# Optimization experiments

Hardware: AMD Instinct MI355X
Metric: run time of the kernel (lower is better)

## Reference

```python
import jax, jax.numpy as jnp
import numpy as np

NUM_HIDDEN = 128
NUM_IN = 256
NUM_HEADS = 4
B, T, N, K = 4, 32, 96, 30


def setup_inputs() -> dict:
    key = jax.random.key(0)
    ks = jax.random.split(key, 7)
    return {
        "h_V": jax.random.normal(ks[0], (B, T, N, NUM_HIDDEN), dtype=jnp.float32),
        "h_EV": jax.random.normal(ks[1], (B, T, N, K, NUM_IN), dtype=jnp.float32),
        "mask_attend": jax.random.randint(ks[2], (B, T, N, K), 0, 2, dtype=jnp.int32),
        "Wq": jax.random.normal(ks[3], (NUM_HIDDEN, NUM_HIDDEN), dtype=jnp.float32) / np.sqrt(NUM_HIDDEN),
        "Wk": jax.random.normal(ks[4], (NUM_IN, NUM_HIDDEN), dtype=jnp.float32) / np.sqrt(NUM_IN),
        "Wv": jax.random.normal(ks[5], (NUM_IN, NUM_HIDDEN), dtype=jnp.float32) / np.sqrt(NUM_IN),
        "Wo": jax.random.normal(ks[6], (NUM_HIDDEN, NUM_HIDDEN), dtype=jnp.float32) / np.sqrt(NUM_HIDDEN),
    }


def reference(h_V, h_EV, mask_attend, Wq, Wk, Wv, Wo):
    b, t, n, k = h_EV.shape[:4]
    h = NUM_HEADS
    d = NUM_HIDDEN // h
    # projections
    Q = (h_V @ Wq).reshape(b, t, n, h, d)            # [B,T,N,H,d]
    Kp = (h_EV @ Wk).reshape(b, t, n, k, h, d)       # [B,T,N,K,H,d]
    V = (h_EV @ Wv).reshape(b, t, n, k, h, d)        # [B,T,N,K,H,d]
    # per-node neighbor attention logits [B,T,N,H,K]
    logits = jnp.einsum('btnhd,btnkhd->btnhk', Q, Kp) / jnp.sqrt(jnp.float32(d))
    neg_inf = jnp.finfo(jnp.float32).min
    mask = mask_attend[:, :, :, None, :]             # [B,T,N,1,K] -> broadcast over heads
    logits = jnp.where(mask > 0, logits, neg_inf)
    attend = jax.nn.softmax(logits, axis=-1)
    attend = attend * mask.astype(jnp.float32)
    # combine values: [B,T,N,H,d]
    out = jnp.einsum('btnhk,btnkhd->btnhd', attend, V).reshape(b, t, n, NUM_HIDDEN)
    return out @ Wo
```

## Files before the change

### kernel.cpp

```cpp
#include <hip/hip_runtime.h>
#include <hip/hip_bf16.h>
#include <cfloat>
#include <math.h>

constexpr int SITES = 12288;
constexpr int KNB   = 30;
constexpr int CIN   = 256;
#define RSQRT_D 0.17677669529663689f

typedef short bf16x8 __attribute__((ext_vector_type(8)));
typedef float f32x4  __attribute__((ext_vector_type(4)));

__device__ inline unsigned short f2bs(float x) {
    __hip_bfloat16 b = __float2bfloat16(x);
    return *(unsigned short*)&b;
}
__device__ inline float bs2f(unsigned short u) {
    unsigned int v = (unsigned int)u << 16;
    float f;
    __builtin_memcpy(&f, &v, 4);
    return f;
}
__device__ inline unsigned int pack2(float a, float b) {
    return (unsigned int)f2bs(a) | ((unsigned int)f2bs(b) << 16);
}

__global__ __launch_bounds__(256) void precompute_w(
    const float* __restrict__ Wq, const float* __restrict__ Wk,
    const float* __restrict__ Wv, const float* __restrict__ Wo,
    unsigned short* __restrict__ Mt, unsigned short* __restrict__ W3t) {
    int gid = blockIdx.x * 256 + threadIdx.x;
    if (gid < 131072) {
        int p = gid >> 7;
        int i = gid & 127;
        int h = p >> 8;
        int c = p & 255;
        const float4* wq = (const float4*)(Wq + (size_t)i * 128 + h * 32);
        const float4* wk = (const float4*)(Wk + (size_t)c * 128 + h * 32);
        float s = 0.f;
        #pragma unroll
        for (int d = 0; d < 8; ++d) {
            float4 a = wq[d], b = wk[d];
            s += a.x * b.x; s += a.y * b.y; s += a.z * b.z; s += a.w * b.w;
        }
        Mt[gid] = f2bs(s);
    } else {
        int o = gid - 131072;
        int p = o >> 7;
        int j = o & 127;
        int h = p >> 8;
        int c = p & 255;
        const float* wv = Wv + (size_t)c * 128 + h * 32;
        const float* wo = Wo + (size_t)(h * 32) * 128 + j;
        float s = 0.f;
        #pragma unroll
        for (int d = 0; d < 32; ++d)
            s += wv[d] * wo[(size_t)d * 128];
        W3t[(size_t)j * 1024 + p] = f2bs(s);
    }
}

template <bool OUT_BF16, bool A_F32>
__global__ __launch_bounds__(256) void gemm_bt_bf16(
    const void* __restrict__ Aptr, const unsigned short* __restrict__ Bt,
    void* __restrict__ C, int M, int N, int K) {
    constexpr int BM = 64, BN = 128, BK = 32, PAD = 8;
    constexpr int NT = BN / 16;
    __shared__ unsigned short As[BM][BK + PAD];
    __shared__ unsigned short Bs[BN][BK + PAD];
    const int tid  = threadIdx.x;
    const int wave = tid >> 6;
    const int lane = tid & 63;
    const int quad = lane >> 4;
    const int l16  = lane & 15;
    const int bm0 = blockIdx.x * BM;
    const int bn0 = blockIdx.y * BN;

    f32x4 acc[NT];
    #pragma unroll
    for (int j = 0; j < NT; ++j) acc[j] = (f32x4){0.f, 0.f, 0.f, 0.f};

    for (int kk = 0; kk < K; kk += BK) {
        {
            int row = tid >> 2, off = (tid & 3) * 8;
            if (A_F32) {
                const float* Af = (const float*)Aptr;
                const float4* src = (const float4*)&Af[(size_t)(bm0 + row) * K + kk + off];
                float4 a0 = src[0], a1 = src[1];
                uint4 p;
                p.x = pack2(a0.x, a0.y); p.y = pack2(a0.z, a0.w);
                p.z = pack2(a1.x, a1.y); p.w = pack2(a1.z, a1.w);
                *(uint4*)&As[row][off] = p;
            } else {
                const unsigned short* Ab = (const unsigned short*)Aptr;
                *(uint4*)&As[row][off] =
                    *(const uint4*)&Ab[(size_t)(bm0 + row) * K + kk + off];
            }
        }
        #pragma unroll
        for (int i = 0; i < 2; ++i) {
            int c2 = tid * 2 + i;
            int brow = c2 >> 2, boff = (c2 & 3) * 8;
            *(uint4*)&Bs[brow][boff] =
                *(const uint4*)&Bt[(size_t)(bn0 + brow) * K + kk + boff];
        }
        __syncthreads();
        bf16x8 af = *(const bf16x8*)&As[wave * 16 + l16][quad * 8];
        #pragma unroll
        for (int j = 0; j < NT; ++j) {
            bf16x8 bf = *(const bf16x8*)&Bs[j * 16 + l16][quad * 8];
            acc[j] = __builtin_amdgcn_mfma_f32_16x16x32_bf16(af, bf, acc[j], 0, 0, 0);
        }
        __syncthreads();
    }
    int row0 = bm0 + wave * 16 + quad * 4;
    #pragma unroll
    for (int j = 0; j < NT; ++j) {
        int col = bn0 + j * 16 + l16;
        #pragma unroll
        for (int r = 0; r < 4; ++r) {
            if (OUT_BF16)
                ((unsigned short*)C)[(size_t)(row0 + r) * N + col] = f2bs(acc[j][r]);
            else
                ((float*)C)[(size_t)(row0 + r) * N + col] = acc[j][r];
        }
    }
}

__global__ __launch_bounds__(256) void attn_out_fused(
    const float* __restrict__ hEV, const int* __restrict__ mask,
    const unsigned short* __restrict__ qt, const unsigned short* __restrict__ W3t,
    float* __restrict__ out) {
    __shared__ __align__(16) unsigned short evbS[16 * 1024];
    const int tid  = threadIdx.x;
    const int lane = tid & 63;
    const int wv   = tid >> 6;
    const int s0   = blockIdx.x * 16;

    for (int si = 0; si < 4; ++si) {
        const int site = wv * 4 + si;
        const int s = s0 + site;

        int mk = (lane < KNB) ? mask[(size_t)s * KNB + lane] : 0;
        unsigned long long bal = __ballot(mk > 0);
        unsigned mw = (unsigned)bal & 0x3FFFFFFFu;
        int na = __popc(mw);

        float qf[4][4];
        const unsigned short* qrow = qt + (size_t)s * 1024;
        #pragma unroll
        for (int h = 0; h < 4; ++h) {
            ushort4 u = *(const ushort4*)&qrow[h * 256 + lane * 4];
            qf[h][0] = bs2f(u.x); qf[h][1] = bs2f(u.y);
            qf[h][2] = bs2f(u.z); qf[h][3] = bs2f(u.w);
        }

        float mh[4], lh[4], acc[4][4];
        #pragma unroll
        for (int h = 0; h < 4; ++h) {
            mh[h] = -3.0e38f; lh[h] = 0.f;
            acc[h][0] = acc[h][1] = acc[h][2] = acc[h][3] = 0.f;
        }

        const float* base = hEV + (size_t)s * (KNB * CIN) + lane * 4;
        unsigned lmw = mw;
        float4 cur = {0,0,0,0}, nxt = {0,0,0,0};
        if (na > 0) {
            int k = __builtin_ctz(lmw); lmw &= lmw - 1;
            cur = *(const float4*)(base + (size_t)k * CIN);
        }
        for (int r = 0; r < na; ++r) {
            if (r + 1 < na) {
                int kn = __builtin_ctz(lmw); lmw &= lmw - 1;
                nxt = *(const float4*)(base + (size_t)kn * CIN);
            }
            float4 v = cur;
            float lg[4];
            #pragma unroll
            for (int h = 0; h < 4; ++h)
                lg[h] = v.x * qf[h][0] + v.y * qf[h][1]
                      + v.z * qf[h][2] + v.w * qf[h][3];
            #pragma unroll
            for (int mm = 1; mm < 64; mm <<= 1) {
                #pragma unroll
                for (int h = 0; h < 4; ++h) lg[h] += __shfl_xor(lg[h], mm, 64);
            }
            #pragma unroll
            for (int h = 0; h < 4; ++h) {
                float g = lg[h] * RSQRT_D;
                if (g > mh[h] + 8.f) {
                    float sc = __expf(mh[h] - g);
                    lh[h] *= sc;
                    acc[h][0] *= sc; acc[h][1] *= sc;
                    acc[h][2] *= sc; acc[h][3] *= sc;
                    mh[h] = g;
                }
                float p = __expf(g - mh[h]);
                lh[h] += p;
                acc[h][0] = fmaf(p, v.x, acc[h][0]);
                acc[h][1] = fmaf(p, v.y, acc[h][1]);
                acc[h][2] = fmaf(p, v.z, acc[h][2]);
                acc[h][3] = fmaf(p, v.w, acc[h][3]);
            }
            cur = nxt;
        }
        const int swz = (site & 7) << 4;
        #pragma unroll
        for (int h = 0; h < 4; ++h) {
            float inv = (lh[h] > 0.f) ? 1.f / lh[h] : 0.f;
            unsigned p0 = pack2(acc[h][0] * inv, acc[h][1] * inv);
            unsigned p1 = pack2(acc[h][2] * inv, acc[h][3] * inv);
            int byte = (h * 512 + lane * 8) ^ swz;
            *(uint2*)((char*)evbS + site * 2048 + byte) = make_uint2(p0, p1);
        }
    }
    __syncthreads();

    const int quad = lane >> 4;
    const int l16  = lane & 15;
    const int n0   = wv * 32;
    f32x4 oacc0 = (f32x4){0.f, 0.f, 0.f, 0.f};
    f32x4 oacc1 = (f32x4){0.f, 0.f, 0.f, 0.f};
    const int aswz = (l16 & 7) << 4;
    #pragma unroll 4
    for (int kk = 0; kk < 1024; kk += 32) {
        int abyte = ((kk + quad * 8) * 2) ^ aswz;
        bf16x8 af = *(const bf16x8*)((const char*)evbS + l16 * 2048 + abyte);
        bf16x8 b0 = *(const bf16x8*)&W3t[(size_t)(n0 + l16) * 1024 + kk + quad * 8];
        bf16x8 b1 = *(const bf16x8*)&W3t[(size_t)(n0 + 16 + l16) * 1024 + kk + quad * 8];
        oacc0 = __builtin_amdgcn_mfma_f32_16x16x32_bf16(af, b0, oacc0, 0, 0, 0);
        oacc1 = __builtin_amdgcn_mfma_f32_16x16x32_bf16(af, b1, oacc1, 0, 0, 0);
    }
    int srow = s0 + quad * 4;
    #pragma unroll
    for (int r = 0; r < 4; ++r) {
        out[(size_t)(srow + r) * 128 + n0 + l16]      = oacc0[r];
        out[(size_t)(srow + r) * 128 + n0 + 16 + l16] = oacc1[r];
    }
}

extern "C" void kernel_launch(void* const* d_in, const int* in_sizes, int n_in,
                              void* d_out, int out_size, void* d_ws, size_t ws_size,
                              hipStream_t stream) {
    const float* hV   = (const float*)d_in[0];
    const float* hEV  = (const float*)d_in[1];
    const int*   mask = (const int*)d_in[2];
    const float* Wq   = (const float*)d_in[3];
    const float* Wk   = (const float*)d_in[4];
    const float* Wv   = (const float*)d_in[5];
    const float* Wo   = (const float*)d_in[6];
    float* out = (float*)d_out;

    unsigned short* ws = (unsigned short*)d_ws;
    unsigned short* Mt   = ws;
    unsigned short* W3t  = ws + 131072;
    unsigned short* qt   = ws + 262144;
    size_t need = ((size_t)262144 + (size_t)SITES * 1024) * 2;
    if (ws_size < need) return;

    precompute_w<<<dim3(1024), dim3(256), 0, stream>>>(Wq, Wk, Wv, Wo, Mt, W3t);

    gemm_bt_bf16<true, true><<<dim3(SITES / 64, 1024 / 128), dim3(256), 0, stream>>>(
        hV, Mt, qt, SITES, 1024, 128);

    attn_out_fused<<<dim3(SITES / 16), dim3(256), 0, stream>>>(
        hEV, mask, qt, W3t, out);
}
```

Measured before the change: 524.0 us.

## Fuse Q projection into attention kernel and remap lanes per head

Computes the hV×Mt projection inside the attention kernel via MFMA into shared memory, removing the separate GEMM launch and the bf16 qt workspace round trip. Reassigns lanes so each 16-lane group owns one head with 16 channels per lane, shrinking the logit reduction from a 64-lane butterfly over four heads to a 16-lane butterfly over one. Increases shared memory per block and register pressure, which may reduce occupancy.

Result: slower. 581.4 us (+11.0%).

```diff
diff --git a/kernel.cpp b/kernel.cpp
--- a/kernel.cpp
+++ b/kernel.cpp
@@ -60,165 +60,142 @@
     }
 }
 
-template <bool OUT_BF16, bool A_F32>
-__global__ __launch_bounds__(256) void gemm_bt_bf16(
-    const void* __restrict__ Aptr, const unsigned short* __restrict__ Bt,
-    void* __restrict__ C, int M, int N, int K) {
-    constexpr int BM = 64, BN = 128, BK = 32, PAD = 8;
-    constexpr int NT = BN / 16;
-    __shared__ unsigned short As[BM][BK + PAD];
-    __shared__ unsigned short Bs[BN][BK + PAD];
-    const int tid  = threadIdx.x;
-    const int wave = tid >> 6;
-    const int lane = tid & 63;
-    const int quad = lane >> 4;
-    const int l16  = lane & 15;
-    const int bm0 = blockIdx.x * BM;
-    const int bn0 = blockIdx.y * BN;
-
-    f32x4 acc[NT];
-    #pragma unroll
-    for (int j = 0; j < NT; ++j) acc[j] = (f32x4){0.f, 0.f, 0.f, 0.f};
-
-    for (int kk = 0; kk < K; kk += BK) {
-        {
-            int row = tid >> 2, off = (tid & 3) * 8;
-            if (A_F32) {
-                const float* Af = (const float*)Aptr;
-                const float4* src = (const float4*)&Af[(size_t)(bm0 + row) * K + kk + off];
-                float4 a0 = src[0], a1 = src[1];
-                uint4 p;
-                p.x = pack2(a0.x, a0.y); p.y = pack2(a0.z, a0.w);
-                p.z = pack2(a1.x, a1.y); p.w = pack2(a1.z, a1.w);
-                *(uint4*)&As[row][off] = p;
-            } else {
-                const unsigned short* Ab = (const unsigned short*)Aptr;
-                *(uint4*)&As[row][off] =
-                    *(const uint4*)&Ab[(size_t)(bm0 + row) * K + kk + off];
-            }
-        }
-        #pragma unroll
-        for (int i = 0; i < 2; ++i) {
-            int c2 = tid * 2 + i;
-            int brow = c2 >> 2, boff = (c2 & 3) * 8;
-            *(uint4*)&Bs[brow][boff] =
-                *(const uint4*)&Bt[(size_t)(bn0 + brow) * K + kk + boff];
-        }
-        __syncthreads();
-        bf16x8 af = *(const bf16x8*)&As[wave * 16 + l16][quad * 8];
-        #pragma unroll
-        for (int j = 0; j < NT; ++j) {
-            bf16x8 bf = *(const bf16x8*)&Bs[j * 16 + l16][quad * 8];
-            acc[j] = __builtin_amdgcn_mfma_f32_16x16x32_bf16(af, bf, acc[j], 0, 0, 0);
-        }
-        __syncthreads();
-    }
-    int row0 = bm0 + wave * 16 + quad * 4;
-    #pragma unroll
-    for (int j = 0; j < NT; ++j) {
-        int col = bn0 + j * 16 + l16;
-        #pragma unroll
-        for (int r = 0; r < 4; ++r) {
-            if (OUT_BF16)
-                ((unsigned short*)C)[(size_t)(row0 + r) * N + col] = f2bs(acc[j][r]);
-            else
-                ((float*)C)[(size_t)(row0 + r) * N + col] = acc[j][r];
-        }
-    }
-}
-
-__global__ __launch_bounds__(256) void attn_out_fused(
-    const float* __restrict__ hEV, const int* __restrict__ mask,
-    const unsigned short* __restrict__ qt, const unsigned short* __restrict__ W3t,
-    float* __restrict__ out) {
+__global__ __launch_bounds__(256) void mega_fused(
+    const float* __restrict__ hV, const float* __restrict__ hEV,
+    const int* __restrict__ mask, const unsigned short* __restrict__ Mt,
+    const unsigned short* __restrict__ W3t, float* __restrict__ out) {
+    __shared__ __align__(16) unsigned short hVs[16][136];
+    __shared__ __align__(16) unsigned short qS[16][1024];
     __shared__ __align__(16) unsigned short evbS[16 * 1024];
     const int tid  = threadIdx.x;
     const int lane = tid & 63;
     const int wv   = tid >> 6;
+    const int quad = lane >> 4;
+    const int l16  = lane & 15;
     const int s0   = blockIdx.x * 16;
 
+    {
+        const float4* src = (const float4*)(hV + (size_t)s0 * 128);
+        float4 a = src[tid * 2], b = src[tid * 2 + 1];
+        int site = tid >> 4, ch = (tid & 15) * 8;
+        uint4 p;
+        p.x = pack2(a.x, a.y); p.y = pack2(a.z, a.w);
+        p.z = pack2(b.x, b.y); p.w = pack2(b.z, b.w);
+        *(uint4*)&hVs[site][ch] = p;
+    }
+    __syncthreads();
+
+    {
+        const int n0 = wv * 256;
+        f32x4 qa[16];
+        #pragma unroll
+        for (int j = 0; j < 16; ++j) qa[j] = (f32x4){0.f, 0.f, 0.f, 0.f};
+        #pragma unroll
+        for (int ks = 0; ks < 4; ++ks) {
+            bf16x8 af = *(const bf16x8*)&hVs[l16][ks * 32 + quad * 8];
+            #pragma unroll
+            for (int j = 0; j < 16; ++j) {
+                bf16x8 bfr = *(const bf16x8*)&Mt[(size_t)(n0 + j * 16 + l16) * 128
+                                                 + ks * 32 + quad * 8];
+                qa[j] = __builtin_amdgcn_mfma_f32_16x16x32_bf16(af, bfr, qa[j], 0, 0, 0);
+            }
+        }
+        #pragma unroll
+        for (int j = 0; j < 16; ++j) {
+            int col = n0 + j * 16 + l16;
+            #pragma unroll
+            for (int r = 0; r < 4; ++r) qS[quad * 4 + r][col] = f2bs(qa[j][r]);
+        }
+    }
+    __syncthreads();
+
+    const int h = lane >> 4;
+    const int g = lane & 15;
     for (int si = 0; si < 4; ++si) {
         const int site = wv * 4 + si;
         const int s = s0 + site;
 
         int mk = (lane < KNB) ? mask[(size_t)s * KNB + lane] : 0;
-        unsigned long long bal = __ballot(mk > 0);
-        unsigned mw = (unsigned)bal & 0x3FFFFFFFu;
+        unsigned mw = (unsigned)__ballot(mk > 0) & 0x3FFFFFFFu;
         int na = __popc(mw);
 
-        float qf[4][4];
-        const unsigned short* qrow = qt + (size_t)s * 1024;
-        #pragma unroll
-        for (int h = 0; h < 4; ++h) {
-            ushort4 u = *(const ushort4*)&qrow[h * 256 + lane * 4];
-            qf[h][0] = bs2f(u.x); qf[h][1] = bs2f(u.y);
-            qf[h][2] = bs2f(u.z); qf[h][3] = bs2f(u.w);
-        }
-
-        float mh[4], lh[4], acc[4][4];
-        #pragma unroll
-        for (int h = 0; h < 4; ++h) {
-            mh[h] = -3.0e38f; lh[h] = 0.f;
-            acc[h][0] = acc[h][1] = acc[h][2] = acc[h][3] = 0.f;
-        }
-
-        const float* base = hEV + (size_t)s * (KNB * CIN) + lane * 4;
+        float qf[16];
+        {
+            const unsigned short* qr = &qS[site][h * 256 + g * 16];
+            bf16x8 q0 = *(const bf16x8*)qr;
+            bf16x8 q1 = *(const bf16x8*)(qr + 8);
+            #pragma unroll
+            for (int j = 0; j < 8; ++j) {
+                qf[j]     = bs2f((unsigned short)q0[j]);
+                qf[8 + j] = bs2f((unsigned short)q1[j]);
+            }
+        }
+
+        float mh = -3.0e38f, lh = 0.f, acc[16];
+        #pragma unroll
+        for (int j = 0; j < 16; ++j) acc[j] = 0.f;
+
+        const float* base = hEV + (size_t)s * (KNB * CIN) + g * 16;
         unsigned lmw = mw;
-        float4 cur = {0,0,0,0}, nxt = {0,0,0,0};
+        float4 cur[4], nxt[4];
         if (na > 0) {
             int k = __builtin_ctz(lmw); lmw &= lmw - 1;
-            cur = *(const float4*)(base + (size_t)k * CIN);
+            const float* rp = base + (size_t)k * CIN;
+            #pragma unroll
+            for (int j = 0; j < 4; ++j) cur[j] = *(const float4*)(rp + j * 4);
         }
         for (int r = 0; r < na; ++r) {
             if (r + 1 < na) {
                 int kn = __builtin_ctz(lmw); lmw &= lmw - 1;
-                nxt = *(const float4*)(base + (size_t)kn * CIN);
-            }
-            float4 v = cur;
-            float lg[4];
-            #pragma unroll
-            for (int h = 0; h < 4; ++h)
-                lg[h] = v.x * qf[h][0] + v.y * qf[h][1]
-                      + v.z * qf[h][2] + v.w * qf[h][3];
-            #pragma unroll
-            for (int mm = 1; mm < 64; mm <<= 1) {
+                const float* rp = base + (size_t)kn * CIN;
                 #pragma unroll
-                for (int h = 0; h < 4; ++h) lg[h] += __shfl_xor(lg[h], mm, 64);
-            }
-            #pragma unroll
-            for (int h = 0; h < 4; ++h) {
-                float g = lg[h] * RSQRT_D;
-                if (g > mh[h] + 8.f) {
-                    float sc = __expf(mh[h] - g);
-                    lh[h] *= sc;
-                    acc[h][0] *= sc; acc[h][1] *= sc;
-                    acc[h][2] *= sc; acc[h][3] *= sc;
-                    mh[h] = g;
-                }
-                float p = __expf(g - mh[h]);
-                lh[h] += p;
-                acc[h][0] = fmaf(p, v.x, acc[h][0]);
-                acc[h][1] = fmaf(p, v.y, acc[h][1]);
-                acc[h][2] = fmaf(p, v.z, acc[h][2]);
-                acc[h][3] = fmaf(p, v.w, acc[h][3]);
-            }
-            cur = nxt;
-        }
+                for (int j = 0; j < 4; ++j) nxt[j] = *(const float4*)(rp + j * 4);
+            }
+            float lg = 0.f;
+            #pragma unroll
+            for (int j = 0; j < 4; ++j) {
+                lg = fmaf(cur[j].x, qf[j * 4 + 0], lg);
+                lg = fmaf(cur[j].y, qf[j * 4 + 1], lg);
+                lg = fmaf(cur[j].z, qf[j * 4 + 2], lg);
+                lg = fmaf(cur[j].w, qf[j * 4 + 3], lg);
+            }
+            lg += __shfl_xor(lg, 1, 64);
+            lg += __shfl_xor(lg, 2, 64);
+            lg += __shfl_xor(lg, 4, 64);
+            lg += __shfl_xor(lg, 8, 64);
+            float gv = lg * RSQRT_D;
+            if (gv > mh + 8.f) {
+                float sc = __expf(mh - gv);
+                lh *= sc;
+                #pragma unroll
+                for (int j = 0; j < 16; ++j) acc[j] *= sc;
+                mh = gv;
+            }
+            float p = __expf(gv - mh);
+            lh += p;
+            #pragma unroll
+            for (int j = 0; j < 4; ++j) {
+                acc[j * 4 + 0] = fmaf(p, cur[j].x, acc[j * 4 + 0]);
+                acc[j * 4 + 1] = fmaf(p, cur[j].y, acc[j * 4 + 1]);
+                acc[j * 4 + 2] = fmaf(p, cur[j].z, acc[j * 4 + 2]);
+                acc[j * 4 + 3] = fmaf(p, cur[j].w, acc[j * 4 + 3]);
+            }
+            #pragma unroll
+            for (int j = 0; j < 4; ++j) cur[j] = nxt[j];
+        }
+        float inv = (lh > 0.f) ? 1.f / lh : 0.f;
+        unsigned pk[8];
+        #pragma unroll
+        for (int j = 0; j < 8; ++j) pk[j] = pack2(acc[2 * j] * inv, acc[2 * j + 1] * inv);
         const int swz = (site & 7) << 4;
-        #pragma unroll
-        for (int h = 0; h < 4; ++h) {
-            float inv = (lh[h] > 0.f) ? 1.f / lh[h] : 0.f;
-            unsigned p0 = pack2(acc[h][0] * inv, acc[h][1] * inv);
-            unsigned p1 = pack2(acc[h][2] * inv, acc[h][3] * inv);
-            int byte = (h * 512 + lane * 8) ^ swz;
-            *(uint2*)((char*)evbS + site * 2048 + byte) = make_uint2(p0, p1);
-        }
+        int b0 = (h * 512 + g * 32) ^ swz;
+        int b1 = (h * 512 + g * 32 + 16) ^ swz;
+        *(uint4*)((char*)evbS + site * 2048 + b0) = make_uint4(pk[0], pk[1], pk[2], pk[3]);
+        *(uint4*)((char*)evbS + site * 2048 + b1) = make_uint4(pk[4], pk[5], pk[6], pk[7]);
     }
     __syncthreads();
 
-    const int quad = lane >> 4;
-    const int l16  = lane & 15;
-    const int n0   = wv * 32;
+    const int n0 = wv * 32;
     f32x4 oacc0 = (f32x4){0.f, 0.f, 0.f, 0.f};
     f32x4 oacc1 = (f32x4){0.f, 0.f, 0.f, 0.f};
     const int aswz = (l16 & 7) << 4;
@@ -254,15 +231,11 @@
     unsigned short* ws = (unsigned short*)d_ws;
     unsigned short* Mt   = ws;
     unsigned short* W3t  = ws + 131072;
-    unsigned short* qt   = ws + 262144;
-    size_t need = ((size_t)262144 + (size_t)SITES * 1024) * 2;
+    size_t need = (size_t)262144 * 2;
     if (ws_size < need) return;
 
     precompute_w<<<dim3(1024), dim3(256), 0, stream>>>(Wq, Wk, Wv, Wo, Mt, W3t);
 
-    gemm_bt_bf16<true, true><<<dim3(SITES / 64, 1024 / 128), dim3(256), 0, stream>>>(
-        hV, Mt, qt, SITES, 1024, 128);
-
-    attn_out_fused<<<dim3(SITES / 16), dim3(256), 0, stream>>>(
-        hEV, mask, qt, W3t, out);
-}
+    mega_fused<<<dim3(SITES / 16), dim3(256), 0, stream>>>(
+        hV, hEV, mask, Mt, W3t, out);
+}
```
